# Kernel tuning notes

Measured on AMD Instinct MI355X. Metric: run time of the kernel, lower is better.

Reference implementation:

```python
import jax, jax.numpy as jnp
import numpy as np

MIN_NORM = 1e-15
PROJ_EPS = 4e-3  # float32 boundary eps used by hgcn PoincareBall.proj
C = 1.0          # curvature for every layer
N, E, D = 10000, 320000, 256


def _norm(x):
    return jnp.maximum(jnp.linalg.norm(x, axis=-1, keepdims=True), MIN_NORM)


def artanh(x):
    return jnp.arctanh(jnp.clip(x, -1 + 1e-7, 1 - 1e-7))


def proj(x, c):
    norm = _norm(x)
    maxnorm = (1.0 - PROJ_EPS) / jnp.sqrt(c)
    return jnp.where(norm > maxnorm, x / norm * maxnorm, x)


def expmap0(u, c):
    sqrt_c = jnp.sqrt(c)
    u_norm = _norm(u)
    return jnp.tanh(sqrt_c * u_norm) * u / (sqrt_c * u_norm)


def logmap0(p, c):
    sqrt_c = jnp.sqrt(c)
    p_norm = _norm(p)
    return artanh(sqrt_c * p_norm) * p / (sqrt_c * p_norm)


def mobius_add(x, y, c):
    x2 = jnp.sum(x * x, -1, keepdims=True)
    y2 = jnp.sum(y * y, -1, keepdims=True)
    xy = jnp.sum(x * y, -1, keepdims=True)
    num = (1 + 2 * c * xy + c * y2) * x + (1 - c * x2) * y
    denom = 1 + 2 * c * xy + c * c * x2 * y2
    return num / jnp.maximum(denom, MIN_NORM)


def mobius_matvec(m, x, c):
    sqrt_c = jnp.sqrt(c)
    x_norm = _norm(x)
    mx = x @ m.T
    mx_norm = _norm(mx)
    res = jnp.tanh(mx_norm / x_norm * artanh(sqrt_c * x_norm)) * mx / (mx_norm * sqrt_c)
    zero_row = jnp.all(mx == 0, axis=-1, keepdims=True)
    return jnp.where(zero_row, jnp.zeros_like(res), res)


def hgc_layer(h, W, b, edge_weight, edge_src, edge_dst, c):
    # HypLinear (dropout=0, eval mode)
    res = proj(mobius_matvec(W, h, c), c)
    hyp_bias = proj(expmap0(b[None, :], c), c)
    h = proj(mobius_add(res, hyp_bias, c), c)
    # HypAgg: tangent-space neighborhood aggregation (spmm over edge list)
    xt = logmap0(h, c)                                  # [N, D]
    msgs = edge_weight[:, None] * xt[edge_src]          # [E, D] irregular gather
    agg = jax.ops.segment_sum(msgs, edge_dst, num_segments=N)
    h = proj(expmap0(agg, c), c)
    # HypAct: relu in tangent space, map back with c_out
    xt = jax.nn.relu(logmap0(h, c))
    return proj(expmap0(xt, c), c)


def setup_inputs() -> dict:
    key = jax.random.key(0)
    ks = jax.random.split(key, 8)
    x = jax.random.normal(ks[0], (N, D), dtype=jnp.float32)
    edge_src = jax.random.randint(ks[1], (E,), 0, N)
    edge_dst = jax.random.randint(ks[2], (E,), 0, N)
    # normalized-adjacency-like positive weights (~1/deg scale)
    edge_weight = jax.random.uniform(ks[3], (E,), dtype=jnp.float32) / 32.0
    s = 1.0 / np.sqrt(D)
    W1 = jax.random.normal(ks[4], (D, D), dtype=jnp.float32) * s
    b1 = jnp.zeros((D,), dtype=jnp.float32)
    W2 = jax.random.normal(ks[5], (D, D), dtype=jnp.float32) * s
    b2 = jnp.zeros((D,), dtype=jnp.float32)
    return {"x": x, "W1": W1, "b1": b1, "W2": W2, "b2": b2,
            "edge_weight": edge_weight, "edge_src": edge_src, "edge_dst": edge_dst}


def reference(x, W1, b1, W2, b2, edge_weight, edge_src, edge_dst):
    # old=True path: map Euclidean features onto the Poincare ball first
    h = proj(expmap0(x, C), C)
    h = hgc_layer(h, W1, b1, edge_weight, edge_src, edge_dst, C)
    h = hgc_layer(h, W2, b2, edge_weight, edge_src, edge_dst, C)
    return h
```

## Files before the change

### kernel.cpp

```cpp
#include <hip/hip_runtime.h>
#include <hip/hip_fp16.h>

#define DIM 256
#define MAXNORM 0.996f
#define MINN 1e-15f
#define CLIPV 0.9999999f

typedef __attribute__((ext_vector_type(8))) short bf16x8;
typedef __attribute__((ext_vector_type(4))) float f32x4;

__device__ __forceinline__ unsigned short f2bf(float f) {
    unsigned int u = __float_as_uint(f);
    u += 0x7fffu + ((u >> 16) & 1u);
    return (unsigned short)(u >> 16);
}
__device__ __forceinline__ float h2f(unsigned short h) {
    return __half2float(__ushort_as_half(h));
}
__device__ __forceinline__ unsigned short f2h(float f) {
    return __half_as_ushort(__float2half(f));
}
__device__ __forceinline__ float wsum(float v) {
    v += __shfl_xor(v, 32);
    v += __shfl_xor(v, 16);
    v += __shfl_xor(v, 8);
    v += __shfl_xor(v, 4);
    v += __shfl_xor(v, 2);
    v += __shfl_xor(v, 1);
    return v;
}

__global__ void k_setup(const float* __restrict__ x, unsigned short* __restrict__ h_bf,
                        float* __restrict__ hnorm2, int nrows,
                        int* __restrict__ csr_off, int nOff,
                        const float* __restrict__ W1, const float* __restrict__ W2,
                        unsigned short* __restrict__ w_bf, int nPerW, int eB) {
    int bid = blockIdx.x;
    if (bid < eB) {
        int gid = bid * 256 + threadIdx.x;
        int row = gid >> 6, lane = gid & 63;
        if (row >= nrows) return;
        size_t base = (size_t)row * DIM + lane * 4;
        float4 v = *(const float4*)(x + base);
        float ss = wsum(v.x * v.x + v.y * v.y + v.z * v.z + v.w * v.w);
        float n = fmaxf(sqrtf(ss), MINN);
        float tn = tanhf(n);
        float hn = (tn > MAXNORM) ? MAXNORM : tn;
        float s = hn / n;
        ushort4 ob;
        ob.x = f2bf(v.x * s); ob.y = f2bf(v.y * s);
        ob.z = f2bf(v.z * s); ob.w = f2bf(v.w * s);
        *(ushort4*)(h_bf + base) = ob;
        if (lane == 0) hnorm2[row] = hn * hn;
    } else if (bid < eB + 64) {
        int i = (bid - eB) * 256 + threadIdx.x;
        int stride = 64 * 256;
        for (; i < nOff; i += stride) csr_off[i] = 0;
    } else {
        int i = (bid - eB - 64) * 256 + threadIdx.x;
        int stride = 128 * 256;
        for (; i < 2 * nPerW; i += stride)
            w_bf[i] = f2bf(i < nPerW ? W1[i] : W2[i - nPerW]);
    }
}

__global__ void k_hist(const int* __restrict__ dst, int* __restrict__ off, int nE, int nrows) {
    int e = blockIdx.x * blockDim.x + threadIdx.x;
    if (e >= nE) return;
    int d = dst[e];
    if (d >= 0 && d < nrows) atomicAdd(&off[d + 1], 1);
}

__global__ void k_scan(int* __restrict__ a, int* __restrict__ cursor, int n) {
    __shared__ int wsums[16];
    int t = threadIdx.x;
    int chunk = (n + 1023) / 1024;
    int lo = t * chunk, hi = min(lo + chunk, n);
    int sum = 0;
    for (int i = lo; i < hi; ++i) sum += a[i];
    int lane = t & 63, wid = t >> 6;
    int v = sum;
    for (int o = 1; o < 64; o <<= 1) {
        int u = __shfl_up(v, o);
        if (lane >= o) v += u;
    }
    if (lane == 63) wsums[wid] = v;
    __syncthreads();
    if (t == 0) {
        int c = 0;
        for (int i = 0; i < 16; ++i) { int x = wsums[i]; wsums[i] = c; c += x; }
    }
    __syncthreads();
    int excl = v - sum + wsums[wid];
    int c = excl;
    for (int i = lo; i < hi; ++i) {
        c += a[i];
        a[i] = c;
        if (i < n - 1) cursor[i] = c;
    }
}

__global__ void k_fill(const int* __restrict__ esrc, const int* __restrict__ edst,
                       const float* __restrict__ ew, int* __restrict__ cursor,
                       int2* __restrict__ csr_pack, int nE, int nrows) {
    int e = blockIdx.x * blockDim.x + threadIdx.x;
    if (e >= nE) return;
    int d = edst[e];
    if (d < 0 || d >= nrows) return;
    int pos = atomicAdd(&cursor[d], 1);
    csr_pack[pos] = make_int2(esrc[e], __float_as_int(ew[e]));
}

__global__ void k_gemm_mfma(const unsigned short* __restrict__ Abf,
                            const unsigned short* __restrict__ Wbf,
                            unsigned short* __restrict__ C16, int M) {
    int wave = threadIdx.x >> 6;
    int lane = threadIdx.x & 63;
    int r = lane & 15, oct = lane >> 4;
    int i0 = blockIdx.y * 64 + wave * 16;
    int j0 = blockIdx.x * 16;
    int arow = i0 + r;
    bool av = arow < M;
    const unsigned short* ap = Abf + (size_t)arow * DIM + oct * 8;
    const unsigned short* bp = Wbf + (size_t)(j0 + r) * DIM + oct * 8;
    const bf16x8 zf = {0, 0, 0, 0, 0, 0, 0, 0};
    f32x4 acc = {0.f, 0.f, 0.f, 0.f};
#pragma unroll
    for (int k0 = 0; k0 < 256; k0 += 32) {
        bf16x8 a = av ? *(const bf16x8*)(ap + k0) : zf;
        bf16x8 b = *(const bf16x8*)(bp + k0);
        acc = __builtin_amdgcn_mfma_f32_16x16x32_bf16(a, b, acc, 0, 0, 0);
    }
#pragma unroll
    for (int q = 0; q < 4; ++q) {
        int row = i0 + oct * 4 + q;
        if (row < M) C16[(size_t)row * DIM + j0 + r] = f2h(acc[q]);
    }
}

__global__ void k_post(const unsigned short* __restrict__ MX16, const float* __restrict__ hnorm2,
                       const float* __restrict__ b, unsigned short* __restrict__ XT, int nrows) {
    int gid = blockIdx.x * blockDim.x + threadIdx.x;
    int row = gid >> 6, lane = gid & 63;
    if (row >= nrows) return;
    size_t base = (size_t)row * DIM + lane * 4;
    ushort4 mu = *(const ushort4*)(MX16 + base);
    float m0 = h2f(mu.x), m1 = h2f(mu.y), m2 = h2f(mu.z), m3 = h2f(mu.w);
    float4 bv = *(const float4*)(b + lane * 4);
    float bs = wsum(bv.x * bv.x + bv.y * bv.y + bv.z * bv.z + bv.w * bv.w);
    float bn = fmaxf(sqrtf(bs), MINN);
    float btn = tanhf(bn);
    float bhn = (btn > MAXNORM) ? MAXNORM : btn;
    float bscale = bhn / bn;
    float e0 = bv.x * bscale, e1 = bv.y * bscale, e2 = bv.z * bscale, e3 = bv.w * bscale;
    float y2 = bhn * bhn;

    float sm = wsum(m0 * m0 + m1 * m1 + m2 * m2 + m3 * m3);
    float sxy = wsum(m0 * e0 + m1 * e1 + m2 * e2 + m3 * e3);
    float sh = hnorm2[row];
    float xn = fmaxf(sqrtf(sh), MINN);
    float at = atanhf(fminf(xn, CLIPV));
    float mn = fmaxf(sqrtf(sm), MINN);
    float t = tanhf(mn / xn * at);
    float alpha = t / mn;
    float resn = t;
    if (t > MAXNORM) { alpha = MAXNORM / mn; resn = MAXNORM; }
    float x2 = resn * resn;
    float xy = alpha * sxy;
    float Aa = 1.f + 2.f * xy + y2;
    float Bb = 1.f - x2;
    float den = fmaxf(1.f + 2.f * xy + x2 * y2, MINN);
    float s_m = Aa * alpha / den;
    float s_b = Bb / den;
    float hn2 = (Aa * Aa * x2 + 2.f * Aa * Bb * xy + Bb * Bb * y2) / (den * den);
    float hn = fmaxf(sqrtf(fmaxf(hn2, 0.f)), MINN);
    if (hn > MAXNORM) { float f = MAXNORM / hn; s_m *= f; s_b *= f; hn = MAXNORM; }
    float lt = atanhf(fminf(hn, CLIPV)) / hn;
    s_m *= lt; s_b *= lt;
    ushort4 o;
    o.x = f2h(s_m * m0 + s_b * e0);
    o.y = f2h(s_m * m1 + s_b * e1);
    o.z = f2h(s_m * m2 + s_b * e2);
    o.w = f2h(s_m * m3 + s_b * e3);
    *(ushort4*)(XT + base) = o;
}

__global__ void k_agg_finish(const unsigned short* __restrict__ XT, const int* __restrict__ off,
                             const int2* __restrict__ cpk,
                             float* __restrict__ OUT, unsigned short* __restrict__ OUT_bf,
                             float* __restrict__ hnorm2, int nrows) {
    int gid = blockIdx.x * blockDim.x + threadIdx.x;
    int row = gid >> 6, lane = gid & 63;
    if (row >= nrows) return;
    int p0 = off[row], p1 = off[row + 1];
    float a0 = 0.f, a1 = 0.f, a2 = 0.f, a3 = 0.f;
    int p = p0;
    for (; p + 7 < p1; p += 8) {
        ushort4 v[8];
        float w[8];
#pragma unroll
        for (int u = 0; u < 8; ++u) {
            int2 pk = cpk[p + u];
            w[u] = __int_as_float(pk.y);
            v[u] = *(const ushort4*)(XT + (size_t)pk.x * DIM + lane * 4);
        }
#pragma unroll
        for (int u = 0; u < 8; ++u) {
            a0 = fmaf(w[u], h2f(v[u].x), a0);
            a1 = fmaf(w[u], h2f(v[u].y), a1);
            a2 = fmaf(w[u], h2f(v[u].z), a2);
            a3 = fmaf(w[u], h2f(v[u].w), a3);
        }
    }
    for (; p < p1; ++p) {
        int2 pk = cpk[p];
        float w = __int_as_float(pk.y);
        ushort4 v = *(const ushort4*)(XT + (size_t)pk.x * DIM + lane * 4);
        a0 = fmaf(w, h2f(v.x), a0); a1 = fmaf(w, h2f(v.y), a1);
        a2 = fmaf(w, h2f(v.z), a2); a3 = fmaf(w, h2f(v.w), a3);
    }
    float ss = wsum(a0 * a0 + a1 * a1 + a2 * a2 + a3 * a3);
    float n = fmaxf(sqrtf(ss), MINN);
    float tn = tanhf(n);
    float hn = (tn > MAXNORM) ? MAXNORM : tn;
    float s1 = hn / n;
    float lt = atanhf(fminf(hn, CLIPV)) / fmaxf(hn, MINN);
    float s2 = lt * s1;
    float x0 = fmaxf(s2 * a0, 0.f), x1 = fmaxf(s2 * a1, 0.f);
    float x2 = fmaxf(s2 * a2, 0.f), x3 = fmaxf(s2 * a3, 0.f);
    float ss2 = wsum(x0 * x0 + x1 * x1 + x2 * x2 + x3 * x3);
    float n2 = fmaxf(sqrtf(ss2), MINN);
    float tn2 = tanhf(n2);
    float hn2c = (tn2 > MAXNORM) ? MAXNORM : tn2;
    float s3 = hn2c / n2;
    float o0 = s3 * x0, o1 = s3 * x1, o2 = s3 * x2, o3 = s3 * x3;
    size_t base = (size_t)row * DIM + lane * 4;
    if (OUT_bf) {
        ushort4 ob;
        ob.x = f2bf(o0); ob.y = f2bf(o1); ob.z = f2bf(o2); ob.w = f2bf(o3);
        *(ushort4*)(OUT_bf + base) = ob;
        if (lane == 0) hnorm2[row] = hn2c * hn2c;
    } else {
        *(float4*)(OUT + base) = make_float4(o0, o1, o2, o3);
    }
}

static inline size_t align256(size_t x) { return (x + 255) & ~(size_t)255; }

extern "C" void kernel_launch(void* const* d_in, const int* in_sizes, int n_in,
                              void* d_out, int out_size, void* d_ws, size_t ws_size,
                              hipStream_t stream) {
    const float* x  = (const float*)d_in[0];
    const float* W1 = (const float*)d_in[1];
    const float* b1 = (const float*)d_in[2];
    const float* W2 = (const float*)d_in[3];
    const float* b2 = (const float*)d_in[4];
    const float* ew = (const float*)d_in[5];
    const int* esrc = (const int*)d_in[6];
    const int* edst = (const int*)d_in[7];
    const int nE = in_sizes[5];
    const int M  = in_sizes[0] / DIM;

    size_t S = (size_t)M * DIM;
    char* base = (char*)d_ws;
    size_t o = 0;
    int2* csr_pack = (int2*)(base + o);          o = align256(o + (size_t)nE * 8);
    int* csr_off   = (int*)(base + o);           o = align256(o + (size_t)(M + 1) * 4);
    int* cursor    = (int*)(base + o);           o = align256(o + (size_t)M * 4);
    float* hnorm2  = (float*)(base + o);         o = align256(o + (size_t)(M + 64) * 4);
    unsigned short* xt   = (unsigned short*)(base + o);  o = align256(o + S * 2);
    unsigned short* h_bf = (unsigned short*)(base + o);  o = align256(o + S * 2);
    unsigned short* mx16 = (unsigned short*)(base + o);  o = align256(o + S * 2);
    unsigned short* w_bf = (unsigned short*)(base + o);  o = align256(o + (size_t)2 * DIM * DIM * 2);

    int rowBlocks = (M + 3) / 4;
    dim3 gemmGrid(DIM / 16, (M + 63) / 64);
    int edgeBlocks = (nE + 255) / 256;

    k_setup<<<rowBlocks + 64 + 128, 256, 0, stream>>>(
        x, h_bf, hnorm2, M, csr_off, M + 1, W1, W2, w_bf, DIM * DIM, rowBlocks);

    k_hist<<<edgeBlocks, 256, 0, stream>>>(edst, csr_off, nE, M);
    k_scan<<<1, 1024, 0, stream>>>(csr_off, cursor, M + 1);
    k_fill<<<edgeBlocks, 256, 0, stream>>>(esrc, edst, ew, cursor, csr_pack, nE, M);

    for (int layer = 0; layer < 2; ++layer) {
        const float* b = (layer == 0) ? b1 : b2;
        const unsigned short* Wb = w_bf + (size_t)layer * DIM * DIM;
        k_gemm_mfma<<<gemmGrid, 256, 0, stream>>>(h_bf, Wb, mx16, M);
        k_post<<<rowBlocks, 256, 0, stream>>>(mx16, hnorm2, b, xt, M);
        k_agg_finish<<<rowBlocks, 256, 0, stream>>>(
            xt, csr_off, csr_pack,
            (layer == 0) ? (float*)nullptr : (float*)d_out,
            (layer == 0) ? h_bf : (unsigned short*)nullptr,
            hnorm2, M);
    }
}
```

Baseline: 242.5 us.

## Fuse MFMA GEMM with hyperbolic post-processing into one full-row kernel

Merges the GEMM and the per-row post-processing (mobius matvec, bias add, proj, logmap0) into a single kernel. Each wave now computes all 256 output columns for 16 rows, with 16 accumulator tiles, so the row norms can be reduced in registers. This removes the fp16 MX intermediate write and read and one kernel launch per layer. The cost is higher register pressure and a much smaller grid (M/64 blocks, about 157), and the XT stores become 2-byte scattered writes.

```diff
diff --git a/kernel.cpp b/kernel.cpp
--- a/kernel.cpp
+++ b/kernel.cpp
@@ -23,6 +23,13 @@
 __device__ __forceinline__ float wsum(float v) {
     v += __shfl_xor(v, 32);
     v += __shfl_xor(v, 16);
+    v += __shfl_xor(v, 8);
+    v += __shfl_xor(v, 4);
+    v += __shfl_xor(v, 2);
+    v += __shfl_xor(v, 1);
+    return v;
+}
+__device__ __forceinline__ float gsum16(float v) {
     v += __shfl_xor(v, 8);
     v += __shfl_xor(v, 4);
     v += __shfl_xor(v, 2);
@@ -111,78 +118,85 @@
     csr_pack[pos] = make_int2(esrc[e], __float_as_int(ew[e]));
 }
 
-__global__ void k_gemm_mfma(const unsigned short* __restrict__ Abf,
+__global__ void k_gemm_post(const unsigned short* __restrict__ Abf,
                             const unsigned short* __restrict__ Wbf,
-                            unsigned short* __restrict__ C16, int M) {
+                            const float* __restrict__ hnorm2,
+                            const float* __restrict__ bias,
+                            unsigned short* __restrict__ XT, int M) {
     int wave = threadIdx.x >> 6;
     int lane = threadIdx.x & 63;
     int r = lane & 15, oct = lane >> 4;
-    int i0 = blockIdx.y * 64 + wave * 16;
-    int j0 = blockIdx.x * 16;
+    int i0 = (blockIdx.x * 4 + wave) * 16;
     int arow = i0 + r;
     bool av = arow < M;
-    const unsigned short* ap = Abf + (size_t)arow * DIM + oct * 8;
-    const unsigned short* bp = Wbf + (size_t)(j0 + r) * DIM + oct * 8;
+    const unsigned short* ap = Abf + (size_t)(av ? arow : 0) * DIM + oct * 8;
+    const unsigned short* wp = Wbf + (size_t)r * DIM + oct * 8;
     const bf16x8 zf = {0, 0, 0, 0, 0, 0, 0, 0};
-    f32x4 acc = {0.f, 0.f, 0.f, 0.f};
-#pragma unroll
+    f32x4 acc[16];
+#pragma unroll
+    for (int jt = 0; jt < 16; ++jt) acc[jt] = (f32x4){0.f, 0.f, 0.f, 0.f};
     for (int k0 = 0; k0 < 256; k0 += 32) {
         bf16x8 a = av ? *(const bf16x8*)(ap + k0) : zf;
-        bf16x8 b = *(const bf16x8*)(bp + k0);
-        acc = __builtin_amdgcn_mfma_f32_16x16x32_bf16(a, b, acc, 0, 0, 0);
-    }
-#pragma unroll
-    for (int q = 0; q < 4; ++q) {
-        int row = i0 + oct * 4 + q;
-        if (row < M) C16[(size_t)row * DIM + j0 + r] = f2h(acc[q]);
-    }
-}
-
-__global__ void k_post(const unsigned short* __restrict__ MX16, const float* __restrict__ hnorm2,
-                       const float* __restrict__ b, unsigned short* __restrict__ XT, int nrows) {
-    int gid = blockIdx.x * blockDim.x + threadIdx.x;
-    int row = gid >> 6, lane = gid & 63;
-    if (row >= nrows) return;
-    size_t base = (size_t)row * DIM + lane * 4;
-    ushort4 mu = *(const ushort4*)(MX16 + base);
-    float m0 = h2f(mu.x), m1 = h2f(mu.y), m2 = h2f(mu.z), m3 = h2f(mu.w);
-    float4 bv = *(const float4*)(b + lane * 4);
-    float bs = wsum(bv.x * bv.x + bv.y * bv.y + bv.z * bv.z + bv.w * bv.w);
-    float bn = fmaxf(sqrtf(bs), MINN);
+#pragma unroll
+        for (int jt = 0; jt < 16; ++jt) {
+            bf16x8 w = *(const bf16x8*)(wp + (size_t)jt * 16 * DIM + k0);
+            acc[jt] = __builtin_amdgcn_mfma_f32_16x16x32_bf16(a, w, acc[jt], 0, 0, 0);
+        }
+    }
+    float bv[16];
+    float bss = 0.f;
+#pragma unroll
+    for (int jt = 0; jt < 16; ++jt) {
+        bv[jt] = bias[jt * 16 + r];
+        bss = fmaf(bv[jt], bv[jt], bss);
+    }
+    bss = gsum16(bss);
+    float bn = fmaxf(sqrtf(bss), MINN);
     float btn = tanhf(bn);
     float bhn = (btn > MAXNORM) ? MAXNORM : btn;
     float bscale = bhn / bn;
-    float e0 = bv.x * bscale, e1 = bv.y * bscale, e2 = bv.z * bscale, e3 = bv.w * bscale;
     float y2 = bhn * bhn;
-
-    float sm = wsum(m0 * m0 + m1 * m1 + m2 * m2 + m3 * m3);
-    float sxy = wsum(m0 * e0 + m1 * e1 + m2 * e2 + m3 * e3);
-    float sh = hnorm2[row];
-    float xn = fmaxf(sqrtf(sh), MINN);
-    float at = atanhf(fminf(xn, CLIPV));
-    float mn = fmaxf(sqrtf(sm), MINN);
-    float t = tanhf(mn / xn * at);
-    float alpha = t / mn;
-    float resn = t;
-    if (t > MAXNORM) { alpha = MAXNORM / mn; resn = MAXNORM; }
-    float x2 = resn * resn;
-    float xy = alpha * sxy;
-    float Aa = 1.f + 2.f * xy + y2;
-    float Bb = 1.f - x2;
-    float den = fmaxf(1.f + 2.f * xy + x2 * y2, MINN);
-    float s_m = Aa * alpha / den;
-    float s_b = Bb / den;
-    float hn2 = (Aa * Aa * x2 + 2.f * Aa * Bb * xy + Bb * Bb * y2) / (den * den);
-    float hn = fmaxf(sqrtf(fmaxf(hn2, 0.f)), MINN);
-    if (hn > MAXNORM) { float f = MAXNORM / hn; s_m *= f; s_b *= f; hn = MAXNORM; }
-    float lt = atanhf(fminf(hn, CLIPV)) / hn;
-    s_m *= lt; s_b *= lt;
-    ushort4 o;
-    o.x = f2h(s_m * m0 + s_b * e0);
-    o.y = f2h(s_m * m1 + s_b * e1);
-    o.z = f2h(s_m * m2 + s_b * e2);
-    o.w = f2h(s_m * m3 + s_b * e3);
-    *(ushort4*)(XT + base) = o;
+#pragma unroll
+    for (int jt = 0; jt < 16; ++jt) bv[jt] *= bscale;
+
+#pragma unroll
+    for (int q = 0; q < 4; ++q) {
+        int row = i0 + oct * 4 + q;
+        float sm = 0.f, sxy = 0.f;
+#pragma unroll
+        for (int jt = 0; jt < 16; ++jt) {
+            float m = acc[jt][q];
+            sm  = fmaf(m, m, sm);
+            sxy = fmaf(m, bv[jt], sxy);
+        }
+        sm = gsum16(sm);
+        sxy = gsum16(sxy);
+        if (row < M) {
+            float sh = hnorm2[row];
+            float xn = fmaxf(sqrtf(sh), MINN);
+            float at = atanhf(fminf(xn, CLIPV));
+            float mn = fmaxf(sqrtf(sm), MINN);
+            float t = tanhf(mn / xn * at);
+            float alpha = t / mn;
+            float resn = t;
+            if (t > MAXNORM) { alpha = MAXNORM / mn; resn = MAXNORM; }
+            float x2 = resn * resn;
+            float xy = alpha * sxy;
+            float Aa = 1.f + 2.f * xy + y2;
+            float Bb = 1.f - x2;
+            float den = fmaxf(1.f + 2.f * xy + x2 * y2, MINN);
+            float s_m = Aa * alpha / den;
+            float s_b = Bb / den;
+            float hn2 = (Aa * Aa * x2 + 2.f * Aa * Bb * xy + Bb * Bb * y2) / (den * den);
+            float hn = fmaxf(sqrtf(fmaxf(hn2, 0.f)), MINN);
+            if (hn > MAXNORM) { float f = MAXNORM / hn; s_m *= f; s_b *= f; hn = MAXNORM; }
+            float lt = atanhf(fminf(hn, CLIPV)) / hn;
+            s_m *= lt; s_b *= lt;
+#pragma unroll
+            for (int jt = 0; jt < 16; ++jt)
+                XT[(size_t)row * DIM + jt * 16 + r] = f2h(fmaf(s_m, acc[jt][q], s_b * bv[jt]));
+        }
+    }
 }
 
 __global__ void k_agg_finish(const unsigned short* __restrict__ XT, const int* __restrict__ off,
@@ -270,11 +284,9 @@
     float* hnorm2  = (float*)(base + o);         o = align256(o + (size_t)(M + 64) * 4);
     unsigned short* xt   = (unsigned short*)(base + o);  o = align256(o + S * 2);
     unsigned short* h_bf = (unsigned short*)(base + o);  o = align256(o + S * 2);
-    unsigned short* mx16 = (unsigned short*)(base + o);  o = align256(o + S * 2);
     unsigned short* w_bf = (unsigned short*)(base + o);  o = align256(o + (size_t)2 * DIM * DIM * 2);
 
     int rowBlocks = (M + 3) / 4;
-    dim3 gemmGrid(DIM / 16, (M + 63) / 64);
     int edgeBlocks = (nE + 255) / 256;
 
     k_setup<<<rowBlocks + 64 + 128, 256, 0, stream>>>(
@@ -287,8 +299,7 @@
     for (int layer = 0; layer < 2; ++layer) {
         const float* b = (layer == 0) ? b1 : b2;
         const unsigned short* Wb = w_bf + (size_t)layer * DIM * DIM;
-        k_gemm_mfma<<<gemmGrid, 256, 0, stream>>>(h_bf, Wb, mx16, M);
-        k_post<<<rowBlocks, 256, 0, stream>>>(mx16, hnorm2, b, xt, M);
+        k_gemm_post<<<(M + 63) / 64, 256, 0, stream>>>(h_bf, Wb, hnorm2, b, xt, M);
         k_agg_finish<<<rowBlocks, 256, 0, stream>>>(
             xt, csr_off, csr_pack,
             (layer == 0) ? (float*)nullptr : (float*)d_out,
```

Result: faster. 230.1 us (-5.1%).
